# Kernel tuning notes

Measured on AMD Instinct MI355X. Metric: run time of the kernel, lower is better.

## Reference

```python
import jax, jax.numpy as jnp
import numpy as np

VOCAB, ATTR, B = 50257, 16, 256
EMB, ATTR_EMB, HID, ZDIM = 300, 200, 700, 500
MAXLEN = 30
SOS_IDX, EOS_IDX = 1, 2


def setup_inputs() -> dict:
    ks = jax.random.split(jax.random.key(0), 8)
    s = 0.02
    return {
        "z": jax.random.normal(ks[0], (B, ZDIM), jnp.float32),
        "l": jax.random.randint(ks[1], (B,), 0, ATTR),
        "emb_w": jax.random.normal(ks[2], (VOCAB, EMB), jnp.float32) * s,
        "attr_w": jax.random.normal(ks[3], (ATTR, ATTR_EMB), jnp.float32) * s,
        "W_ih": jax.random.normal(ks[4], (3 * HID, EMB), jnp.float32) * s,
        "W_hh": jax.random.normal(ks[5], (3 * HID, HID), jnp.float32) * s,
        "b_ih": jnp.zeros((3 * HID,), jnp.float32),
        "b_hh": jnp.zeros((3 * HID,), jnp.float32),
        "out_w": jax.random.normal(ks[6], (VOCAB, HID), jnp.float32) * s,
        "out_b": jnp.zeros((VOCAB,), jnp.float32),
    }


def gru_cell(x, h, W_ih, W_hh, b_ih, b_hh):
    # PyTorch GRU cell: r,z,n gate ordering
    gi = x @ W_ih.T + b_ih          # (B, 3H)
    gh = h @ W_hh.T + b_hh          # (B, 3H)
    i_r, i_z, i_n = jnp.split(gi, 3, axis=-1)
    h_r, h_z, h_n = jnp.split(gh, 3, axis=-1)
    r = jax.nn.sigmoid(i_r + h_r)
    zg = jax.nn.sigmoid(i_z + h_z)
    n = jnp.tanh(i_n + r * h_n)
    return (1.0 - zg) * n + zg * h


def reference(z, l, emb_w, attr_w, W_ih, W_hh, b_ih, b_hh, out_w, out_b):
    # hidden init: cat([z (B,500), attr_emb(l) (B,200)]) -> (B,700)
    h0 = jnp.concatenate([z, attr_w[l]], axis=-1)
    tok0 = jnp.full((B,), SOS_IDX, jnp.int32)
    keys = jax.random.split(jax.random.key(42), MAXLEN)

    def step(carry, k):
        h, tok = carry
        x = emb_w[tok]                                   # (B,300)
        h = gru_cell(x, h, W_ih, W_hh, b_ih, b_hh)       # (B,700)
        logits = h @ out_w.T + out_b                     # (B,VOCAB)
        # multinomial(softmax(logits), 1).detach()
        nxt = jax.lax.stop_gradient(
            jax.random.categorical(k, logits).astype(jnp.int32))
        return (h, nxt), (h, nxt)

    (h_last, _), (hy_t, y_t) = jax.lax.scan(step, (h0, tok0), keys)
    # final forced-EOS step
    eos = jnp.full((B,), EOS_IDX, jnp.int32)
    h_final = gru_cell(emb_w[eos], h_last, W_ih, W_hh, b_ih, b_hh)
    hy = jnp.concatenate([jnp.transpose(hy_t, (1, 0, 2)), h_final[:, None, :]], axis=1)  # (B,MAXLEN+1,700)
    y = jnp.concatenate([jnp.transpose(y_t, (1, 0)), eos[:, None]], axis=1)              # (B,MAXLEN+1)
    return hy, y
```

## Files before the change

kernel.cpp:

```cpp
#include <hip/hip_runtime.h>
#include <stdint.h>

#define VOCAB 50257
#define B 256
#define EMB 300
#define HID 700
#define G3 2100
#define ZDIM 500
#define ATTR_EMBD 200
#define MAXLEN 30
#define SEQ 31
#define HY_ELEMS (B*SEQ*HID)
#define KP 704
#define NKT 22
#define KIH 320
#define VPAD 50304
#define NVT 393
#define MPAD 2112
#define SOS_IDX 1
#define EOS_IDX 2
#define CHUNK 4096
#define TILE_STRIDE ((size_t)NKT * 2 * CHUNK)

typedef _Float16 half8 __attribute__((ext_vector_type(8)));
typedef _Float16 half4 __attribute__((ext_vector_type(4)));
typedef float f32x4 __attribute__((ext_vector_type(4)));

typedef const __attribute__((address_space(1))) void* gas1_t;
typedef __attribute__((address_space(3))) void* las3_t;
__device__ __forceinline__ void gload_lds16(const void* g, void* l) {
  __builtin_amdgcn_global_load_lds((gas1_t)g, (las3_t)l, 16, 0, 0);
}

__device__ __forceinline__ uint32_t rotl32(uint32_t x, int r) {
  return (x << r) | (x >> (32 - r));
}

__device__ __forceinline__ void threefry2x32(uint32_t k0, uint32_t k1,
                                             uint32_t x0, uint32_t x1,
                                             uint32_t& o0, uint32_t& o1) {
  const uint32_t ks2 = k0 ^ k1 ^ 0x1BD11BDAu;
  x0 += k0; x1 += k1;
#define TF_R4(a, b, c, d)                                     \
  x0 += x1; x1 = rotl32(x1, a); x1 ^= x0;                     \
  x0 += x1; x1 = rotl32(x1, b); x1 ^= x0;                     \
  x0 += x1; x1 = rotl32(x1, c); x1 ^= x0;                     \
  x0 += x1; x1 = rotl32(x1, d); x1 ^= x0;
  TF_R4(13, 15, 26, 6)  x0 += k1;  x1 += ks2 + 1u;
  TF_R4(17, 29, 16, 24) x0 += ks2; x1 += k0 + 2u;
  TF_R4(13, 15, 26, 6)  x0 += k0;  x1 += k1 + 3u;
  TF_R4(17, 29, 16, 24) x0 += k1;  x1 += ks2 + 4u;
  TF_R4(13, 15, 26, 6)  x0 += ks2; x1 += k0 + 5u;
#undef TF_R4
  o0 = x0; o1 = x1;
}

__device__ __forceinline__ unsigned long long gumbel_pack(float s, uint32_t key0,
                                                          uint32_t key1, int b, int v) {
  uint32_t j = (uint32_t)(b * VOCAB + v);
  uint32_t o0, o1;
  threefry2x32(key0, key1, 0u, j, o0, o1);
  uint32_t bits = o0 ^ o1;
  float f = __uint_as_float((bits >> 9) | 0x3f800000u) - 1.0f;
  float u = fmaxf(f, 1.17549435e-38f);
  float g = -logf(-logf(u));
  s += g;
  uint32_t us = __float_as_uint(s);
  us = (us & 0x80000000u) ? ~us : (us | 0x80000000u);
  return ((unsigned long long)us << 32) | (uint32_t)(~(uint32_t)v);
}

struct hl16 { _Float16 hi, lo; };
__device__ __forceinline__ hl16 split16(float val, float scale) {
  float s = val * scale;
  _Float16 h = (_Float16)s;
  hl16 r;
  r.hi = h;
  r.lo = (_Float16)((s - (float)h) * 2048.0f);
  return r;
}

__global__ void k_init(const float* __restrict__ z, const int* __restrict__ l,
                       const float* __restrict__ attr_w, const float* __restrict__ emb_w,
                       float* __restrict__ hbuf0, uint32_t* __restrict__ keys,
                       unsigned long long* __restrict__ slots,
                       int* __restrict__ tok, float* __restrict__ y_out,
                       _Float16* __restrict__ h_hi, _Float16* __restrict__ h_lo,
                       _Float16* __restrict__ ht,
                       _Float16* __restrict__ x0_hi, _Float16* __restrict__ x0_lo,
                       _Float16* __restrict__ xe_hi, _Float16* __restrict__ xe_lo,
                       int full) {
  int idx = blockIdx.x * blockDim.x + threadIdx.x;
  if (idx < B * HID) {
    int b = idx / HID, i = idx % HID;
    float v = (i < ZDIM) ? z[b * ZDIM + i]
                         : attr_w[l[b] * ATTR_EMBD + (i - ZDIM)];
    hbuf0[idx] = v;
    hl16 r = split16(v, 8.0f);
    h_hi[b * KP + i] = r.hi;
    h_lo[b * KP + i] = r.lo;
  }
  if (idx < MAXLEN) {
    uint32_t o0, o1;
    threefry2x32(0u, 42u, 0u, (uint32_t)idx, o0, o1);
    keys[2 * idx] = o0; keys[2 * idx + 1] = o1;
  }
  if (idx < MAXLEN * B) slots[idx] = 0ull;
  if (idx < B) {
    tok[idx] = SOS_IDX;
    tok[31 * B + idx] = EOS_IDX;
    y_out[idx * SEQ + MAXLEN] = 2.0f;
  }
  if (idx < B * 4) {
    int b = idx >> 2, k = HID + (idx & 3);
    h_hi[b * KP + k] = (_Float16)0.0f;
    h_lo[b * KP + k] = (_Float16)0.0f;
    int c = b >> 7, row = b & 127, e = k & 7;
    size_t tb = (size_t)c * TILE_STRIDE + (size_t)21 * 2 * CHUNK
              + (3 * 128 + row) * 8 + e;
    ht[tb] = (_Float16)0.0f;
    ht[tb + CHUNK] = (_Float16)0.0f;
  }
  if (full && idx < KIH) {
    float v0 = (idx < EMB) ? emb_w[SOS_IDX * EMB + idx] : 0.0f;
    float ve = (idx < EMB) ? emb_w[EOS_IDX * EMB + idx] : 0.0f;
    hl16 r0 = split16(v0, 8.0f);
    hl16 re = split16(ve, 8.0f);
    for (int b = 0; b < B; ++b) {
      x0_hi[b * KIH + idx] = r0.hi; x0_lo[b * KIH + idx] = r0.lo;
      xe_hi[b * KIH + idx] = re.hi; xe_lo[b * KIH + idx] = re.lo;
    }
  }
}

__global__ void k_wsplit(const float* __restrict__ out_w, _Float16* __restrict__ wt) {
  size_t idx = (size_t)blockIdx.x * blockDim.x + threadIdx.x;
  if (idx >= (size_t)NVT * NKT * 1024) return;
  int h4 = (int)(idx & 1023);
  int ktp = (int)(idx >> 10);
  int kt = ktp % NKT, p = ktp / NKT;
  int slot4 = h4 >> 1, e0 = (h4 & 1) * 4;
  int kc = slot4 >> 7, row = slot4 & 127;
  int v = p * 128 + row;
  int k = kt * 32 + kc * 8 + e0;
  float x[4];
  if (v < VOCAB && k + 3 < HID) {
    const float4 xv = *(const float4*)&out_w[(size_t)v * HID + k];
    x[0] = xv.x; x[1] = xv.y; x[2] = xv.z; x[3] = xv.w;
  } else {
#pragma unroll
    for (int j = 0; j < 4; ++j)
      x[j] = (v < VOCAB && k + j < HID) ? out_w[(size_t)v * HID + k + j] : 0.0f;
  }
  half4 hi, lo;
#pragma unroll
  for (int j = 0; j < 4; ++j) {
    hl16 r = split16(x[j], 64.0f);
    hi[j] = r.hi; lo[j] = r.lo;
  }
  size_t base = (size_t)p * TILE_STRIDE + (size_t)kt * 2 * CHUNK + slot4 * 8 + e0;
  *(half4*)&wt[base] = hi;
  *(half4*)&wt[base + CHUNK] = lo;
}

__global__ void k_gwsplit(const float* __restrict__ src, _Float16* __restrict__ hi,
                          _Float16* __restrict__ lo, int Msrc, int Ksrc, int Kpad,
                          int tot4) {
  int idx = blockIdx.x * blockDim.x + threadIdx.x;
  if (idx >= tot4) return;
  size_t i4 = (size_t)idx * 4;
  int m = (int)(i4 / Kpad), k = (int)(i4 % Kpad);
  half4 h, l;
#pragma unroll
  for (int j = 0; j < 4; ++j) {
    float x = (m < Msrc && k + j < Ksrc) ? src[(size_t)m * Ksrc + k + j] : 0.0f;
    hl16 r = split16(x, 64.0f);
    h[j] = r.hi; l[j] = r.lo;
  }
  *(half4*)&hi[i4] = h;
  *(half4*)&lo[i4] = l;
}

__global__ __launch_bounds__(256, 4)
void k_gates2(const _Float16* __restrict__ wih_hi, const _Float16* __restrict__ wih_lo,
              const _Float16* __restrict__ whh_hi, const _Float16* __restrict__ whh_lo,
              const _Float16* __restrict__ x_hi, const _Float16* __restrict__ x_lo,
              const _Float16* __restrict__ h_hi, const _Float16* __restrict__ h_lo,
              float* __restrict__ gi, float* __restrict__ gh) {
  const int zz = blockIdx.z;
  const _Float16* __restrict__ Whi = zz ? whh_hi : wih_hi;
  const _Float16* __restrict__ Wlo = zz ? whh_lo : wih_lo;
  const _Float16* __restrict__ Xhi = zz ? h_hi : x_hi;
  const _Float16* __restrict__ Xlo = zz ? h_lo : x_lo;
  const int Kz = zz ? KP : KIH;
  float* __restrict__ out = zz ? gh : gi;

  const int jbase = blockIdx.x * 64;
  const int bbase = blockIdx.y * 64;
  __shared__ float4 lds[2][4][256];
  const int tid = threadIdx.x, lane = tid & 63, wid = tid >> 6;
  const int wj = wid >> 1, wb2 = wid & 1;
  const size_t wrow = (size_t)(jbase + lane) * Kz;
  const size_t xrow = (size_t)(bbase + lane) * Kz;

  f32x4 acc_h[2][2], acc_x[2][2];
#pragma unroll
  for (int i = 0; i < 2; ++i)
#pragma unroll
    for (int j = 0; j < 2; ++j) { acc_h[i][j] = (f32x4)0.0f; acc_x[i][j] = (f32x4)0.0f; }

#define GSTAGE(bf, k0)                                                   \
  {                                                                      \
    gload_lds16(Whi + wrow + (k0) + wid * 8, &lds[bf][0][wid * 64]);     \
    gload_lds16(Wlo + wrow + (k0) + wid * 8, &lds[bf][1][wid * 64]);     \
    gload_lds16(Xhi + xrow + (k0) + wid * 8, &lds[bf][2][wid * 64]);     \
    gload_lds16(Xlo + xrow + (k0) + wid * 8, &lds[bf][3][wid * 64]);     \
  }

  const int nt = Kz / 32;
  GSTAGE(0, 0)
  for (int kt = 0; kt < nt; ++kt) {
    const int cur = kt & 1;
    __syncthreads();
    if (kt + 1 < nt) GSTAGE(cur ^ 1, (kt + 1) * 32)
    const int kcf = (lane >> 4) * 64 + (lane & 15);
    half8 a_hi[2], a_lo[2];
#pragma unroll
    for (int fv = 0; fv < 2; ++fv) {
      int s = kcf + wj * 32 + fv * 16;
      a_hi[fv] = *(const half8*)&lds[cur][0][s];
      a_lo[fv] = *(const half8*)&lds[cur][1][s];
    }
#pragma unroll
    for (int fb = 0; fb < 2; ++fb) {
      int s = kcf + wb2 * 32 + fb * 16;
      half8 b_hi = *(const half8*)&lds[cur][2][s];
      half8 b_lo = *(const half8*)&lds[cur][3][s];
#pragma unroll
      for (int fv = 0; fv < 2; ++fv) {
        acc_h[fv][fb] = __builtin_amdgcn_mfma_f32_16x16x32_f16(a_hi[fv], b_hi,
                                                               acc_h[fv][fb], 0, 0, 0);
        acc_x[fv][fb] = __builtin_amdgcn_mfma_f32_16x16x32_f16(a_hi[fv], b_lo,
                                                               acc_x[fv][fb], 0, 0, 0);
        acc_x[fv][fb] = __builtin_amdgcn_mfma_f32_16x16x32_f16(a_lo[fv], b_hi,
                                                               acc_x[fv][fb], 0, 0, 0);
      }
    }
  }
#undef GSTAGE

  const float c1 = 1.0f / 2048.0f, c2 = 1.0f / 512.0f;
#pragma unroll
  for (int fb = 0; fb < 2; ++fb) {
    const int b = bbase + wb2 * 32 + fb * 16 + (lane & 15);
#pragma unroll
    for (int fv = 0; fv < 2; ++fv) {
#pragma unroll
      for (int r = 0; r < 4; ++r) {
        int j = jbase + wj * 32 + fv * 16 + (lane >> 4) * 4 + r;
        if (j < G3)
          out[b * G3 + j] = (acc_h[fv][fb][r] + acc_x[fv][fb][r] * c1) * c2;
      }
    }
  }
}

__global__ void k_gates(const float* __restrict__ W_ih, const float* __restrict__ W_hh,
                        const float* __restrict__ emb_w, const float* __restrict__ hprev,
                        const int* __restrict__ tok,
                        float* __restrict__ gi, float* __restrict__ gh) {
  const int zz = blockIdx.z;
  const float* __restrict__ W = zz ? W_hh : W_ih;
  const int K = zz ? HID : EMB;
  float* __restrict__ out = zz ? gh : gi;
  __shared__ float w_lds[20][36];
  __shared__ float xh_lds[20][36];
  const int jbase = blockIdx.x * 32;
  const int bbase = blockIdx.y * 32;
  const int tid = threadIdx.x;
  const int tj = tid % 16, tb = tid / 16;
  float a00 = 0.f, a01 = 0.f, a10 = 0.f, a11 = 0.f;
  for (int k0 = 0; k0 < K; k0 += 20) {
    for (int idx = tid; idx < 640; idx += 256) {
      int col = idx / 20, kk = idx % 20;
      int j = jbase + col;
      w_lds[kk][col] = (j < G3) ? W[j * K + k0 + kk] : 0.0f;
      int b = bbase + col;
      float xv;
      if (zz) xv = hprev[b * HID + k0 + kk];
      else    xv = emb_w[tok[b] * EMB + k0 + kk];
      xh_lds[kk][col] = xv;
    }
    __syncthreads();
#pragma unroll
    for (int kk = 0; kk < 20; ++kk) {
      float w0 = w_lds[kk][tj * 2], w1 = w_lds[kk][tj * 2 + 1];
      float h0 = xh_lds[kk][tb * 2], h1 = xh_lds[kk][tb * 2 + 1];
      a00 += w0 * h0; a01 += w0 * h1;
      a10 += w1 * h0; a11 += w1 * h1;
    }
    __syncthreads();
  }
  int j0 = jbase + tj * 2, b0 = bbase + tb * 2;
  if (j0 < G3)     { out[b0 * G3 + j0] = a00;     out[(b0 + 1) * G3 + j0] = a01; }
  if (j0 + 1 < G3) { out[b0 * G3 + j0 + 1] = a10; out[(b0 + 1) * G3 + j0 + 1] = a11; }
}

__global__ void k_hnew(const float* __restrict__ gi, const float* __restrict__ gh,
                       const float* __restrict__ b_ih, const float* __restrict__ b_hh,
                       const float* __restrict__ hprev, float* __restrict__ hnext,
                       float* __restrict__ hy, _Float16* __restrict__ h_hi,
                       _Float16* __restrict__ h_lo, _Float16* __restrict__ ht, int t) {
  int idx = blockIdx.x * blockDim.x + threadIdx.x;
  if (idx >= B * HID) return;
  int b = idx / HID, i = idx % HID;
  float ir = gi[b * G3 + i]            + b_ih[i];
  float iz = gi[b * G3 + HID + i]      + b_ih[HID + i];
  float in_ = gi[b * G3 + 2 * HID + i] + b_ih[2 * HID + i];
  float hr = gh[b * G3 + i]            + b_hh[i];
  float hz = gh[b * G3 + HID + i]      + b_hh[HID + i];
  float hn = gh[b * G3 + 2 * HID + i]  + b_hh[2 * HID + i];
  float r  = 1.0f / (1.0f + expf(-(ir + hr)));
  float zg = 1.0f / (1.0f + expf(-(iz + hz)));
  float n  = tanhf(in_ + r * hn);
  float h  = (1.0f - zg) * n + zg * hprev[idx];
  hnext[idx] = h;
  hy[(size_t)b * SEQ * HID + (size_t)t * HID + i] = h;
  hl16 rr = split16(h, 8.0f);
  h_hi[b * KP + i] = rr.hi;
  h_lo[b * KP + i] = rr.lo;
  int c = b >> 7, row = b & 127;
  size_t tb = (size_t)c * TILE_STRIDE + (size_t)(i >> 5) * 2 * CHUNK
            + ((((i >> 3) & 3) * 128 + row) * 8) + (i & 7);
  ht[tb] = rr.hi;
  ht[tb + CHUNK] = rr.lo;
}

__global__ __launch_bounds__(256, 2)
void k_logits2(const _Float16* __restrict__ wt, const _Float16* __restrict__ ht,
               const float* __restrict__ out_b, const uint32_t* __restrict__ keys,
               unsigned long long* __restrict__ slot, int t) {
  const int bid = blockIdx.x;
  const int xcd = bid & 7, li = bid >> 3;
  const int p = xcd * 50 + (li >> 1);
  if (p >= NVT) return;
  const int c = li & 1;
  const int vbase = p * 128, bbase = c * 128;

  __shared__ float4 lds[2][4][512];
  const int tid = threadIdx.x;
  const int lane = tid & 63;
  const int wid = tid >> 6;
  const int wv = wid >> 1, wb = wid & 1;

  const int part = wid & 1;
  const _Float16* tile_base = (wid < 2) ? (wt + (size_t)p * TILE_STRIDE)
                                        : (ht + (size_t)c * TILE_STRIDE);

  f32x4 acc_h[4][4];
  f32x4 acc_x[4][4];
#pragma unroll
  for (int i = 0; i < 4; ++i)
#pragma unroll
    for (int j = 0; j < 4; ++j) { acc_h[i][j] = (f32x4)0.0f; acc_x[i][j] = (f32x4)0.0f; }

#define LSTAGE(bf, kt)                                                          \
  {                                                                             \
    const _Float16* sb =                                                        \
        tile_base + ((size_t)(kt) * 2 + part) * CHUNK + lane * 8;               \
    _Pragma("unroll")                                                           \
    for (int i = 0; i < 8; ++i)                                                 \
      gload_lds16(sb + i * 512, &lds[bf][wid][i * 64]);                         \
  }

  LSTAGE(0, 0)
  for (int kt = 0; kt < NKT; ++kt) {
    const int cur = kt & 1;
    __syncthreads();
    if (kt + 1 < NKT) LSTAGE(cur ^ 1, kt + 1)
    const int kcf = (lane >> 4) * 128 + (lane & 15);
    half8 a_hi[4], a_lo[4];
#pragma unroll
    for (int fv = 0; fv < 4; ++fv) {
      int s = kcf + wv * 64 + fv * 16;
      a_hi[fv] = *(const half8*)&lds[cur][0][s];
      a_lo[fv] = *(const half8*)&lds[cur][1][s];
    }
#pragma unroll
    for (int fb = 0; fb < 4; ++fb) {
      int s = kcf + wb * 64 + fb * 16;
      half8 b_hi = *(const half8*)&lds[cur][2][s];
      half8 b_lo = *(const half8*)&lds[cur][3][s];
#pragma unroll
      for (int fv = 0; fv < 4; ++fv) {
        acc_h[fv][fb] = __builtin_amdgcn_mfma_f32_16x16x32_f16(a_hi[fv], b_hi,
                                                               acc_h[fv][fb], 0, 0, 0);
        acc_x[fv][fb] = __builtin_amdgcn_mfma_f32_16x16x32_f16(a_hi[fv], b_lo,
                                                               acc_x[fv][fb], 0, 0, 0);
        acc_x[fv][fb] = __builtin_amdgcn_mfma_f32_16x16x32_f16(a_lo[fv], b_hi,
                                                               acc_x[fv][fb], 0, 0, 0);
      }
    }
  }
#undef LSTAGE

  const uint32_t key0 = keys[2 * t], key1 = keys[2 * t + 1];
  const float c1 = 1.0f / 2048.0f, c2 = 1.0f / 512.0f;
#pragma unroll
  for (int fb = 0; fb < 4; ++fb) {
    const int b = bbase + wb * 64 + fb * 16 + (lane & 15);
    unsigned long long best = 0ull;
#pragma unroll
    for (int fv = 0; fv < 4; ++fv) {
#pragma unroll
      for (int r = 0; r < 4; ++r) {
        int v = vbase + wv * 64 + fv * 16 + (lane >> 4) * 4 + r;
        if (v < VOCAB) {
          float s = (acc_h[fv][fb][r] + acc_x[fv][fb][r] * c1) * c2 + out_b[v];
          unsigned long long cand = gumbel_pack(s, key0, key1, b, v);
          if (cand > best) best = cand;
        }
      }
    }
    unsigned long long o;
    o = __shfl_xor(best, 16, 64); if (o > best) best = o;
    o = __shfl_xor(best, 32, 64); if (o > best) best = o;
    if ((lane >> 4) == 0) atomicMax(&slot[b], best);
  }
}

#define WPITCH 68
#define HPITCH 260
__global__ __launch_bounds__(256)
void k_logits_f32(const float* __restrict__ h, const float* __restrict__ out_w,
                  const float* __restrict__ out_b, const uint32_t* __restrict__ keys,
                  unsigned long long* __restrict__ slot, int t) {
  __shared__ float w_lds[20][WPITCH];
  __shared__ float h_lds[20][HPITCH];
  const int vbase = blockIdx.x * 64;
  const int tid = threadIdx.x;
  const int tv = tid % 8, tb = tid / 8;
  float acc[8][8];
#pragma unroll
  for (int i = 0; i < 8; ++i)
#pragma unroll
    for (int j = 0; j < 8; ++j) acc[i][j] = 0.f;

  for (int k0 = 0; k0 < HID; k0 += 20) {
    for (int idx = tid; idx < 64 * 20; idx += 256) {
      int vv = idx / 20, kk = idx % 20;
      int v = vbase + vv;
      w_lds[kk][vv] = (v < VOCAB) ? out_w[(size_t)v * HID + k0 + kk] : 0.0f;
    }
    for (int idx = tid; idx < 256 * 20; idx += 256) {
      int bb = idx / 20, kk = idx % 20;
      h_lds[kk][bb] = h[bb * HID + k0 + kk];
    }
    __syncthreads();
#pragma unroll
    for (int kk = 0; kk < 20; ++kk) {
      float wv[8], hv[8];
      *(float4*)&wv[0] = *(const float4*)&w_lds[kk][tv * 8];
      *(float4*)&wv[4] = *(const float4*)&w_lds[kk][tv * 8 + 4];
      *(float4*)&hv[0] = *(const float4*)&h_lds[kk][tb * 8];
      *(float4*)&hv[4] = *(const float4*)&h_lds[kk][tb * 8 + 4];
#pragma unroll
      for (int iv = 0; iv < 8; ++iv)
#pragma unroll
        for (int ib = 0; ib < 8; ++ib) acc[iv][ib] += wv[iv] * hv[ib];
    }
    __syncthreads();
  }

  const uint32_t key0 = keys[2 * t], key1 = keys[2 * t + 1];
#pragma unroll
  for (int ib = 0; ib < 8; ++ib) {
    const int b = tb * 8 + ib;
    unsigned long long best = 0ull;
#pragma unroll
    for (int iv = 0; iv < 8; ++iv) {
      int v = vbase + tv * 8 + iv;
      if (v >= VOCAB) continue;
      unsigned long long cand = gumbel_pack(acc[iv][ib] + out_b[v], key0, key1, b, v);
      if (cand > best) best = cand;
    }
#pragma unroll
    for (int off = 1; off < 8; off <<= 1) {
      unsigned long long other = __shfl_xor(best, off, 64);
      if (other > best) best = other;
    }
    if (tv == 0) atomicMax(&slot[b], best);
  }
}

__global__ void k_tok2(const unsigned long long* __restrict__ slot,
                       const float* __restrict__ emb_w,
                       int* __restrict__ tok_next, float* __restrict__ y_out,
                       _Float16* __restrict__ xc_hi, _Float16* __restrict__ xc_lo,
                       int t, int full) {
  const int b = blockIdx.x;
  const int c = threadIdx.x;
  unsigned long long p = slot[b];
  uint32_t v = ~((uint32_t)(p & 0xFFFFFFFFull));
  if (c == 0) {
    tok_next[b] = (int)v;
    y_out[b * SEQ + t] = (float)v;
  }
  if (!full) return;
  if (c < 75) {
    float4 xv = *(const float4*)&emb_w[(size_t)v * EMB + c * 4];
    half4 hi, lo;
    hl16 r0 = split16(xv.x, 8.0f); hi[0] = r0.hi; lo[0] = r0.lo;
    hl16 r1 = split16(xv.y, 8.0f); hi[1] = r1.hi; lo[1] = r1.lo;
    hl16 r2 = split16(xv.z, 8.0f); hi[2] = r2.hi; lo[2] = r2.lo;
    hl16 r3 = split16(xv.w, 8.0f); hi[3] = r3.hi; lo[3] = r3.lo;
    *(half4*)&xc_hi[b * KIH + c * 4] = hi;
    *(half4*)&xc_lo[b * KIH + c * 4] = lo;
  } else if (c < 80) {
    *(half4*)&xc_hi[b * KIH + c * 4] = (half4)(_Float16)0.0f;
    *(half4*)&xc_lo[b * KIH + c * 4] = (half4)(_Float16)0.0f;
  }
}

extern "C" void kernel_launch(void* const* d_in, const int* in_sizes, int n_in,
                              void* d_out, int out_size, void* d_ws, size_t ws_size,
                              hipStream_t stream) {
  const float* z      = (const float*)d_in[0];
  const int*   l      = (const int*)  d_in[1];
  const float* emb_w  = (const float*)d_in[2];
  const float* attr_w = (const float*)d_in[3];
  const float* W_ih   = (const float*)d_in[4];
  const float* W_hh   = (const float*)d_in[5];
  const float* b_ih   = (const float*)d_in[6];
  const float* b_hh   = (const float*)d_in[7];
  const float* out_w  = (const float*)d_in[8];
  const float* out_b  = (const float*)d_in[9];

  float* hy    = (float*)d_out;
  float* y_out = (float*)d_out + HY_ELEMS;

  char* ws = (char*)d_ws;
  size_t off = 0;
  uint32_t* keys            = (uint32_t*)(ws + off);           off += 256;
  unsigned long long* slots = (unsigned long long*)(ws + off); off += (size_t)MAXLEN * B * 8;
  int* tokbuf               = (int*)(ws + off);                off += (size_t)32 * B * 4;
  float* hbuf               = (float*)(ws + off);              off += (size_t)2 * B * HID * 4;
  float* gi                 = (float*)(ws + off);              off += (size_t)B * G3 * 4;
  float* gh                 = (float*)(ws + off);              off += (size_t)B * G3 * 4;
  _Float16* h_hi            = (_Float16*)(ws + off);           off += (size_t)B * KP * 2;
  _Float16* h_lo            = (_Float16*)(ws + off);           off += (size_t)B * KP * 2;
  _Float16* ht              = (_Float16*)(ws + off);           off += (size_t)2 * TILE_STRIDE * 2;
  _Float16* wt              = (_Float16*)(ws + off);           off += (size_t)NVT * TILE_STRIDE * 2;
  const size_t tier1_end = off;
  _Float16* wih_hi          = (_Float16*)(ws + off);           off += (size_t)MPAD * KIH * 2;
  _Float16* wih_lo          = (_Float16*)(ws + off);           off += (size_t)MPAD * KIH * 2;
  _Float16* whh_hi          = (_Float16*)(ws + off);           off += (size_t)MPAD * KP * 2;
  _Float16* whh_lo          = (_Float16*)(ws + off);           off += (size_t)MPAD * KP * 2;
  _Float16* x0_hi           = (_Float16*)(ws + off);           off += (size_t)B * KIH * 2;
  _Float16* x0_lo           = (_Float16*)(ws + off);           off += (size_t)B * KIH * 2;
  _Float16* xe_hi           = (_Float16*)(ws + off);           off += (size_t)B * KIH * 2;
  _Float16* xe_lo           = (_Float16*)(ws + off);           off += (size_t)B * KIH * 2;
  _Float16* xc_hi           = (_Float16*)(ws + off);           off += (size_t)B * KIH * 2;
  _Float16* xc_lo           = (_Float16*)(ws + off);           off += (size_t)B * KIH * 2;
  const size_t tier2_end = off;
  const int tier = (ws_size >= tier2_end) ? 2 : ((ws_size >= tier1_end) ? 1 : 0);

  k_init<<<(B * HID + 255) / 256, 256, 0, stream>>>(
      z, l, attr_w, emb_w, hbuf, keys, slots, tokbuf, y_out, h_hi, h_lo, ht,
      x0_hi, x0_lo, xe_hi, xe_lo, (tier == 2) ? 1 : 0);

  if (tier >= 1) {
    size_t tot = (size_t)NVT * NKT * 1024;
    k_wsplit<<<(int)((tot + 255) / 256), 256, 0, stream>>>(out_w, wt);
  }
  if (tier == 2) {
    int tih = MPAD * KIH / 4, thh = MPAD * KP / 4;
    k_gwsplit<<<(tih + 255) / 256, 256, 0, stream>>>(W_ih, wih_hi, wih_lo, G3, EMB, KIH, tih);
    k_gwsplit<<<(thh + 255) / 256, 256, 0, stream>>>(W_hh, whh_hi, whh_lo, G3, HID, KP, thh);
  }

  for (int t = 0; t <= MAXLEN; ++t) {
    float* hprev = hbuf + (t % 2) * B * HID;
    float* hnext = hbuf + ((t + 1) % 2) * B * HID;

    if (tier == 2) {
      const _Float16* xh = (t == 0) ? x0_hi : ((t == MAXLEN) ? xe_hi : xc_hi);
      const _Float16* xl = (t == 0) ? x0_lo : ((t == MAXLEN) ? xe_lo : xc_lo);
      dim3 g2(33, 4, 2);
      k_gates2<<<g2, 256, 0, stream>>>(wih_hi, wih_lo, whh_hi, whh_lo,
                                       xh, xl, h_hi, h_lo, gi, gh);
    } else {
      const int* tok_t = tokbuf + ((t == MAXLEN) ? 31 : t) * B;
      dim3 ggrid(66, 8, 2);
      k_gates<<<ggrid, 256, 0, stream>>>(W_ih, W_hh, emb_w, hprev, tok_t, gi, gh);
    }
    k_hnew<<<(B * HID + 255) / 256, 256, 0, stream>>>(gi, gh, b_ih, b_hh, hprev,
                                                      hnext, hy, h_hi, h_lo, ht, t);
    if (t < MAXLEN) {
      if (tier >= 1) {
        k_logits2<<<800, 256, 0, stream>>>(wt, ht, out_b, keys,
                                           slots + (size_t)t * B, t);
      } else {
        k_logits_f32<<<(VOCAB + 63) / 64, 256, 0, stream>>>(hnext, out_w, out_b, keys,
                                                            slots + (size_t)t * B, t);
      }
      k_tok2<<<B, 128, 0, stream>>>(slots + (size_t)t * B, emb_w,
                                    tokbuf + (t + 1) * B, y_out, xc_hi, xc_lo,
                                    t, (tier == 2) ? 1 : 0);
    }
  }
}
```

Measured before the change: 4.025 ms.

## Load logits MFMA operands directly from global into registers, drop LDS staging

The logits GEMM kernel stops staging weight and hidden tiles through double-buffered shared memory with per-iteration block barriers. Each wave now loads its own A and B fragments straight from global memory into registers, ping-ponging two register sets for the weight fragments to overlap loads with MFMA work. This removes the LDS round trip and the __syncthreads per k-tile. The cost is redundant global and L2 loads across waves, since each weight fragment is read by two waves and each h fragment by two, and higher register pressure that may hurt occupancy.

```diff
diff --git a/kernel.cpp b/kernel.cpp
--- a/kernel.cpp
+++ b/kernel.cpp
@@ -337,7 +337,7 @@
 }
 
 __global__ __launch_bounds__(256, 2)
-void k_logits2(const _Float16* __restrict__ wt, const _Float16* __restrict__ ht,
+void k_logits3(const _Float16* __restrict__ wt, const _Float16* __restrict__ ht,
                const float* __restrict__ out_b, const uint32_t* __restrict__ keys,
                unsigned long long* __restrict__ slot, int t) {
   const int bid = blockIdx.x;
@@ -347,15 +347,16 @@
   const int c = li & 1;
   const int vbase = p * 128, bbase = c * 128;
 
-  __shared__ float4 lds[2][4][512];
   const int tid = threadIdx.x;
   const int lane = tid & 63;
   const int wid = tid >> 6;
   const int wv = wid >> 1, wb = wid & 1;
 
-  const int part = wid & 1;
-  const _Float16* tile_base = (wid < 2) ? (wt + (size_t)p * TILE_STRIDE)
-                                        : (ht + (size_t)c * TILE_STRIDE);
+  const _Float16* __restrict__ wp = wt + (size_t)p * TILE_STRIDE;
+  const _Float16* __restrict__ hp = ht + (size_t)c * TILE_STRIDE;
+  const int kcf = (lane >> 4) * 128 + (lane & 15);
+  const int aoff = (kcf + wv * 64) * 8;
+  const int boff = (kcf + wb * 64) * 8;
 
   f32x4 acc_h[4][4];
   f32x4 acc_x[4][4];
@@ -364,45 +365,53 @@
 #pragma unroll
     for (int j = 0; j < 4; ++j) { acc_h[i][j] = (f32x4)0.0f; acc_x[i][j] = (f32x4)0.0f; }
 
-#define LSTAGE(bf, kt)                                                          \
-  {                                                                             \
-    const _Float16* sb =                                                        \
-        tile_base + ((size_t)(kt) * 2 + part) * CHUNK + lane * 8;               \
-    _Pragma("unroll")                                                           \
-    for (int i = 0; i < 8; ++i)                                                 \
-      gload_lds16(sb + i * 512, &lds[bf][wid][i * 64]);                         \
-  }
-
-  LSTAGE(0, 0)
-  for (int kt = 0; kt < NKT; ++kt) {
-    const int cur = kt & 1;
-    __syncthreads();
-    if (kt + 1 < NKT) LSTAGE(cur ^ 1, kt + 1)
-    const int kcf = (lane >> 4) * 128 + (lane & 15);
-    half8 a_hi[4], a_lo[4];
-#pragma unroll
-    for (int fv = 0; fv < 4; ++fv) {
-      int s = kcf + wv * 64 + fv * 16;
-      a_hi[fv] = *(const half8*)&lds[cur][0][s];
-      a_lo[fv] = *(const half8*)&lds[cur][1][s];
-    }
-#pragma unroll
-    for (int fb = 0; fb < 4; ++fb) {
-      int s = kcf + wb * 64 + fb * 16;
-      half8 b_hi = *(const half8*)&lds[cur][2][s];
-      half8 b_lo = *(const half8*)&lds[cur][3][s];
-#pragma unroll
-      for (int fv = 0; fv < 4; ++fv) {
-        acc_h[fv][fb] = __builtin_amdgcn_mfma_f32_16x16x32_f16(a_hi[fv], b_hi,
-                                                               acc_h[fv][fb], 0, 0, 0);
-        acc_x[fv][fb] = __builtin_amdgcn_mfma_f32_16x16x32_f16(a_hi[fv], b_lo,
-                                                               acc_x[fv][fb], 0, 0, 0);
-        acc_x[fv][fb] = __builtin_amdgcn_mfma_f32_16x16x32_f16(a_lo[fv], b_hi,
-                                                               acc_x[fv][fb], 0, 0, 0);
-      }
-    }
-  }
-#undef LSTAGE
+  half8 wA_hi[4], wA_lo[4], wB_hi[4], wB_lo[4], hC_hi[4], hC_lo[4];
+
+#define LOADW(WH, WL, ktv)                                                \
+  {                                                                       \
+    const _Float16* bw = wp + (size_t)(ktv) * (2 * CHUNK);                \
+    _Pragma("unroll")                                                     \
+    for (int fv = 0; fv < 4; ++fv) {                                      \
+      WH[fv] = *(const half8*)(bw + aoff + fv * 128);                     \
+      WL[fv] = *(const half8*)(bw + CHUNK + aoff + fv * 128);             \
+    }                                                                     \
+  }
+#define LOADH(ktv)                                                        \
+  {                                                                       \
+    const _Float16* bh = hp + (size_t)(ktv) * (2 * CHUNK);                \
+    _Pragma("unroll")                                                     \
+    for (int fb = 0; fb < 4; ++fb) {                                      \
+      hC_hi[fb] = *(const half8*)(bh + boff + fb * 128);                  \
+      hC_lo[fb] = *(const half8*)(bh + CHUNK + boff + fb * 128);          \
+    }                                                                     \
+  }
+#define MFMAB(AH, AL)                                                     \
+  _Pragma("unroll")                                                       \
+  for (int fb = 0; fb < 4; ++fb) {                                        \
+    _Pragma("unroll")                                                     \
+    for (int fv = 0; fv < 4; ++fv) {                                      \
+      acc_h[fv][fb] = __builtin_amdgcn_mfma_f32_16x16x32_f16(             \
+          AH[fv], hC_hi[fb], acc_h[fv][fb], 0, 0, 0);                     \
+      acc_x[fv][fb] = __builtin_amdgcn_mfma_f32_16x16x32_f16(             \
+          AH[fv], hC_lo[fb], acc_x[fv][fb], 0, 0, 0);                     \
+      acc_x[fv][fb] = __builtin_amdgcn_mfma_f32_16x16x32_f16(             \
+          AL[fv], hC_hi[fb], acc_x[fv][fb], 0, 0, 0);                     \
+    }                                                                     \
+  }
+
+  LOADW(wA_hi, wA_lo, 0)
+#pragma unroll 1
+  for (int kt = 0; kt < NKT; kt += 2) {
+    LOADH(kt)
+    LOADW(wB_hi, wB_lo, kt + 1)
+    MFMAB(wA_hi, wA_lo)
+    LOADH(kt + 1)
+    if (kt + 2 < NKT) LOADW(wA_hi, wA_lo, kt + 2)
+    MFMAB(wB_hi, wB_lo)
+  }
+#undef LOADW
+#undef LOADH
+#undef MFMAB
 
   const uint32_t key0 = keys[2 * t], key1 = keys[2 * t + 1];
   const float c1 = 1.0f / 2048.0f, c2 = 1.0f / 512.0f;
@@ -598,7 +607,7 @@
                                                       hnext, hy, h_hi, h_lo, ht, t);
     if (t < MAXLEN) {
       if (tier >= 1) {
-        k_logits2<<<800, 256, 0, stream>>>(wt, ht, out_b, keys,
+        k_logits3<<<800, 256, 0, stream>>>(wt, ht, out_b, keys,
                                            slots + (size_t)t * B, t);
       } else {
         k_logits_f32<<<(VOCAB + 63) / 64, 256, 0, stream>>>(hnext, out_w, out_b, keys,
```

Result: slower. 4.125 ms (+2.5%).

## Retile logits GEMM into 128x32 work items with persistent multi-item blocks

Applied to the files above, without the earlier changes.

Replaces the 128x128 vocab-by-batch logits tile kernel with one that processes three 128x32 items per block, staging only weight tiles in LDS while loading the small hidden-state fragments directly from global memory. The hidden-state tile layout is changed to 32-row batch chunks to match, and occupancy is raised to 4 blocks per SM. The Gumbel sampling also switches to fast __logf. Total weight traffic grows because each weight tile is now read once per 32-row batch chunk instead of once per 128-row chunk, which it relies on L2 to absorb. The fast log may change sampled tokens slightly.

```diff
diff --git a/kernel.cpp b/kernel.cpp
--- a/kernel.cpp
+++ b/kernel.cpp
@@ -21,6 +21,10 @@
 #define EOS_IDX 2
 #define CHUNK 4096
 #define TILE_STRIDE ((size_t)NKT * 2 * CHUNK)
+#define HT_KT 2048
+#define HT_C ((size_t)NKT * HT_KT)
+#define NITEMS 3144
+#define NBLK 1048
 
 typedef _Float16 half8 __attribute__((ext_vector_type(8)));
 typedef _Float16 half4 __attribute__((ext_vector_type(4)));
@@ -63,7 +67,7 @@
   uint32_t bits = o0 ^ o1;
   float f = __uint_as_float((bits >> 9) | 0x3f800000u) - 1.0f;
   float u = fmaxf(f, 1.17549435e-38f);
-  float g = -logf(-logf(u));
+  float g = -__logf(-__logf(u));
   s += g;
   uint32_t us = __float_as_uint(s);
   us = (us & 0x80000000u) ? ~us : (us | 0x80000000u);
@@ -115,11 +119,11 @@
     int b = idx >> 2, k = HID + (idx & 3);
     h_hi[b * KP + k] = (_Float16)0.0f;
     h_lo[b * KP + k] = (_Float16)0.0f;
-    int c = b >> 7, row = b & 127, e = k & 7;
-    size_t tb = (size_t)c * TILE_STRIDE + (size_t)21 * 2 * CHUNK
-              + (3 * 128 + row) * 8 + e;
+    int c = b >> 5, row = b & 31;
+    size_t tb = (size_t)c * HT_C + (size_t)21 * HT_KT + (size_t)(3 * 32 + row) * 8
+              + (k & 7);
     ht[tb] = (_Float16)0.0f;
-    ht[tb + CHUNK] = (_Float16)0.0f;
+    ht[tb + 1024] = (_Float16)0.0f;
   }
   if (full && idx < KIH) {
     float v0 = (idx < EMB) ? emb_w[SOS_IDX * EMB + idx] : 0.0f;
@@ -329,104 +333,106 @@
   hl16 rr = split16(h, 8.0f);
   h_hi[b * KP + i] = rr.hi;
   h_lo[b * KP + i] = rr.lo;
-  int c = b >> 7, row = b & 127;
-  size_t tb = (size_t)c * TILE_STRIDE + (size_t)(i >> 5) * 2 * CHUNK
-            + ((((i >> 3) & 3) * 128 + row) * 8) + (i & 7);
+  int c = b >> 5, row = b & 31;
+  size_t tb = (size_t)c * HT_C + (size_t)(i >> 5) * HT_KT
+            + (size_t)((((i >> 3) & 3) * 32 + row) * 8) + (i & 7);
   ht[tb] = rr.hi;
-  ht[tb + CHUNK] = rr.lo;
-}
-
-__global__ __launch_bounds__(256, 2)
-void k_logits2(const _Float16* __restrict__ wt, const _Float16* __restrict__ ht,
+  ht[tb + 1024] = rr.lo;
+}
+
+__global__ __launch_bounds__(256, 4)
+void k_logits4(const _Float16* __restrict__ wt, const _Float16* __restrict__ ht,
                const float* __restrict__ out_b, const uint32_t* __restrict__ keys,
                unsigned long long* __restrict__ slot, int t) {
-  const int bid = blockIdx.x;
-  const int xcd = bid & 7, li = bid >> 3;
-  const int p = xcd * 50 + (li >> 1);
-  if (p >= NVT) return;
-  const int c = li & 1;
-  const int vbase = p * 128, bbase = c * 128;
-
-  __shared__ float4 lds[2][4][512];
+  __shared__ float4 ldsw[2][1024];
   const int tid = threadIdx.x;
   const int lane = tid & 63;
   const int wid = tid >> 6;
-  const int wv = wid >> 1, wb = wid & 1;
-
-  const int part = wid & 1;
-  const _Float16* tile_base = (wid < 2) ? (wt + (size_t)p * TILE_STRIDE)
-                                        : (ht + (size_t)c * TILE_STRIDE);
-
-  f32x4 acc_h[4][4];
-  f32x4 acc_x[4][4];
-#pragma unroll
-  for (int i = 0; i < 4; ++i)
-#pragma unroll
-    for (int j = 0; j < 4; ++j) { acc_h[i][j] = (f32x4)0.0f; acc_x[i][j] = (f32x4)0.0f; }
-
-#define LSTAGE(bf, kt)                                                          \
-  {                                                                             \
-    const _Float16* sb =                                                        \
-        tile_base + ((size_t)(kt) * 2 + part) * CHUNK + lane * 8;               \
-    _Pragma("unroll")                                                           \
-    for (int i = 0; i < 8; ++i)                                                 \
-      gload_lds16(sb + i * 512, &lds[bf][wid][i * 64]);                         \
-  }
-
-  LSTAGE(0, 0)
-  for (int kt = 0; kt < NKT; ++kt) {
-    const int cur = kt & 1;
-    __syncthreads();
-    if (kt + 1 < NKT) LSTAGE(cur ^ 1, kt + 1)
-    const int kcf = (lane >> 4) * 128 + (lane & 15);
-    half8 a_hi[4], a_lo[4];
-#pragma unroll
-    for (int fv = 0; fv < 4; ++fv) {
-      int s = kcf + wv * 64 + fv * 16;
-      a_hi[fv] = *(const half8*)&lds[cur][0][s];
-      a_lo[fv] = *(const half8*)&lds[cur][1][s];
-    }
-#pragma unroll
-    for (int fb = 0; fb < 4; ++fb) {
-      int s = kcf + wb * 64 + fb * 16;
-      half8 b_hi = *(const half8*)&lds[cur][2][s];
-      half8 b_lo = *(const half8*)&lds[cur][3][s];
-#pragma unroll
-      for (int fv = 0; fv < 4; ++fv) {
-        acc_h[fv][fb] = __builtin_amdgcn_mfma_f32_16x16x32_f16(a_hi[fv], b_hi,
-                                                               acc_h[fv][fb], 0, 0, 0);
-        acc_x[fv][fb] = __builtin_amdgcn_mfma_f32_16x16x32_f16(a_hi[fv], b_lo,
-                                                               acc_x[fv][fb], 0, 0, 0);
-        acc_x[fv][fb] = __builtin_amdgcn_mfma_f32_16x16x32_f16(a_lo[fv], b_hi,
-                                                               acc_x[fv][fb], 0, 0, 0);
-      }
-    }
-  }
-#undef LSTAGE
+  const int work = (blockIdx.x & 7) * 131 + (blockIdx.x >> 3);
 
   const uint32_t key0 = keys[2 * t], key1 = keys[2 * t + 1];
   const float c1 = 1.0f / 2048.0f, c2 = 1.0f / 512.0f;
-#pragma unroll
-  for (int fb = 0; fb < 4; ++fb) {
-    const int b = bbase + wb * 64 + fb * 16 + (lane & 15);
-    unsigned long long best = 0ull;
-#pragma unroll
-    for (int fv = 0; fv < 4; ++fv) {
-#pragma unroll
-      for (int r = 0; r < 4; ++r) {
-        int v = vbase + wv * 64 + fv * 16 + (lane >> 4) * 4 + r;
-        if (v < VOCAB) {
-          float s = (acc_h[fv][fb][r] + acc_x[fv][fb][r] * c1) * c2 + out_b[v];
-          unsigned long long cand = gumbel_pack(s, key0, key1, b, v);
-          if (cand > best) best = cand;
+
+  const int wrow = (lane >> 4) * 128 + (lane & 15) + wid * 32;
+  const int hrow = ((lane >> 4) * 32 + (lane & 15)) * 8;
+
+#define STAGE4(bf, ktv)                                                        \
+  {                                                                            \
+    _Pragma("unroll")                                                          \
+    for (int j = 0; j < 4; ++j) {                                              \
+      const int s = wid * 4 + j;                                               \
+      gload_lds16(wp + (size_t)(ktv) * (2 * CHUNK) + (size_t)(s >> 3) * CHUNK  \
+                      + (s & 7) * 512 + lane * 8,                              \
+                  &ldsw[bf][s * 64]);                                          \
+    }                                                                          \
+  }
+
+  for (int it = 0; it < 3; ++it) {
+    const int item = work * 3 + it;
+    const int p = item >> 3, cc = item & 7;
+    const int vbase = p * 128, bbase = cc * 32;
+    const _Float16* __restrict__ wp = wt + (size_t)p * TILE_STRIDE;
+    const _Float16* __restrict__ hq0 = ht + (size_t)cc * HT_C;
+
+    f32x4 acc_h[2][2], acc_x[2][2];
+#pragma unroll
+    for (int i = 0; i < 2; ++i)
+#pragma unroll
+      for (int j = 0; j < 2; ++j) { acc_h[i][j] = (f32x4)0.0f; acc_x[i][j] = (f32x4)0.0f; }
+
+    STAGE4(0, 0)
+    for (int kt = 0; kt < NKT; ++kt) {
+      const int cur = kt & 1;
+      __syncthreads();
+      const _Float16* hq = hq0 + (size_t)kt * HT_KT;
+      half8 hC_hi[2], hC_lo[2];
+      hC_hi[0] = *(const half8*)(hq + hrow);
+      hC_hi[1] = *(const half8*)(hq + hrow + 128);
+      hC_lo[0] = *(const half8*)(hq + 1024 + hrow);
+      hC_lo[1] = *(const half8*)(hq + 1024 + hrow + 128);
+      if (kt + 1 < NKT) STAGE4(cur ^ 1, kt + 1)
+      half8 wA_hi[2], wA_lo[2];
+      wA_hi[0] = *(const half8*)&ldsw[cur][wrow];
+      wA_hi[1] = *(const half8*)&ldsw[cur][wrow + 16];
+      wA_lo[0] = *(const half8*)&ldsw[cur][wrow + 512];
+      wA_lo[1] = *(const half8*)&ldsw[cur][wrow + 512 + 16];
+#pragma unroll
+      for (int fb = 0; fb < 2; ++fb) {
+#pragma unroll
+        for (int fv = 0; fv < 2; ++fv) {
+          acc_h[fv][fb] = __builtin_amdgcn_mfma_f32_16x16x32_f16(
+              wA_hi[fv], hC_hi[fb], acc_h[fv][fb], 0, 0, 0);
+          acc_x[fv][fb] = __builtin_amdgcn_mfma_f32_16x16x32_f16(
+              wA_hi[fv], hC_lo[fb], acc_x[fv][fb], 0, 0, 0);
+          acc_x[fv][fb] = __builtin_amdgcn_mfma_f32_16x16x32_f16(
+              wA_lo[fv], hC_hi[fb], acc_x[fv][fb], 0, 0, 0);
         }
       }
     }
-    unsigned long long o;
-    o = __shfl_xor(best, 16, 64); if (o > best) best = o;
-    o = __shfl_xor(best, 32, 64); if (o > best) best = o;
-    if ((lane >> 4) == 0) atomicMax(&slot[b], best);
-  }
+
+#pragma unroll
+    for (int fb = 0; fb < 2; ++fb) {
+      const int b = bbase + fb * 16 + (lane & 15);
+      unsigned long long best = 0ull;
+#pragma unroll
+      for (int fv = 0; fv < 2; ++fv) {
+#pragma unroll
+        for (int r = 0; r < 4; ++r) {
+          int v = vbase + wid * 32 + fv * 16 + (lane >> 4) * 4 + r;
+          if (v < VOCAB) {
+            float s = (acc_h[fv][fb][r] + acc_x[fv][fb][r] * c1) * c2 + out_b[v];
+            unsigned long long cand = gumbel_pack(s, key0, key1, b, v);
+            if (cand > best) best = cand;
+          }
+        }
+      }
+      unsigned long long o;
+      o = __shfl_xor(best, 16, 64); if (o > best) best = o;
+      o = __shfl_xor(best, 32, 64); if (o > best) best = o;
+      if ((lane >> 4) == 0) atomicMax(&slot[b], best);
+    }
+  }
+#undef STAGE4
 }
 
 #define WPITCH 68
@@ -549,7 +555,7 @@
   float* gh                 = (float*)(ws + off);              off += (size_t)B * G3 * 4;
   _Float16* h_hi            = (_Float16*)(ws + off);           off += (size_t)B * KP * 2;
   _Float16* h_lo            = (_Float16*)(ws + off);           off += (size_t)B * KP * 2;
-  _Float16* ht              = (_Float16*)(ws + off);           off += (size_t)2 * TILE_STRIDE * 2;
+  _Float16* ht              = (_Float16*)(ws + off);           off += (size_t)8 * HT_C * 2;
   _Float16* wt              = (_Float16*)(ws + off);           off += (size_t)NVT * TILE_STRIDE * 2;
   const size_t tier1_end = off;
   _Float16* wih_hi          = (_Float16*)(ws + off);           off += (size_t)MPAD * KIH * 2;
@@ -598,8 +604,8 @@
                                                       hnext, hy, h_hi, h_lo, ht, t);
     if (t < MAXLEN) {
       if (tier >= 1) {
-        k_logits2<<<800, 256, 0, stream>>>(wt, ht, out_b, keys,
-                                           slots + (size_t)t * B, t);
+        k_logits4<<<NBLK, 256, 0, stream>>>(wt, ht, out_b, keys,
+                                            slots + (size_t)t * B, t);
       } else {
         k_logits_f32<<<(VOCAB + 63) / 64, 256, 0, stream>>>(hnext, out_w, out_b, keys,
                                                             slots + (size_t)t * B, t);
```

Measured after the change: 5.136 ms. 1.28x slower.

## Restructure logits GEMM with register-held weights, smaller tiles and single accumulator

Applied to the files above, without the earlier changes.

Replaces the logits kernel with a version that splits each vocab tile into halves across more blocks and keeps weight fragments in registers loaded directly from global memory. Only the hidden-state tile is staged in LDS, with an explicit double buffer. The hi/lo split drops its 2048 scaling so all three MFMA products can accumulate into one register set, halving accumulator pressure and allowing four blocks per CU. Fast __logf replaces logf in the Gumbel sampling. The risks are fp16 underflow of the unscaled low part, which reduces precision, and small deviations from the fast log that could flip sampled tokens.

```diff
diff --git a/kernel.cpp b/kernel.cpp
--- a/kernel.cpp
+++ b/kernel.cpp
@@ -21,6 +21,8 @@
 #define EOS_IDX 2
 #define CHUNK 4096
 #define TILE_STRIDE ((size_t)NKT * 2 * CHUNK)
+#define NIT5 1572
+#define NBLK5 1576
 
 typedef _Float16 half8 __attribute__((ext_vector_type(8)));
 typedef _Float16 half4 __attribute__((ext_vector_type(4)));
@@ -63,7 +65,7 @@
   uint32_t bits = o0 ^ o1;
   float f = __uint_as_float((bits >> 9) | 0x3f800000u) - 1.0f;
   float u = fmaxf(f, 1.17549435e-38f);
-  float g = -logf(-logf(u));
+  float g = -__logf(-__logf(u));
   s += g;
   uint32_t us = __float_as_uint(s);
   us = (us & 0x80000000u) ? ~us : (us | 0x80000000u);
@@ -76,7 +78,7 @@
   _Float16 h = (_Float16)s;
   hl16 r;
   r.hi = h;
-  r.lo = (_Float16)((s - (float)h) * 2048.0f);
+  r.lo = (_Float16)(s - (float)h);
   return r;
 }
 
@@ -203,11 +205,11 @@
   const size_t wrow = (size_t)(jbase + lane) * Kz;
   const size_t xrow = (size_t)(bbase + lane) * Kz;
 
-  f32x4 acc_h[2][2], acc_x[2][2];
+  f32x4 acc[2][2];
 #pragma unroll
   for (int i = 0; i < 2; ++i)
 #pragma unroll
-    for (int j = 0; j < 2; ++j) { acc_h[i][j] = (f32x4)0.0f; acc_x[i][j] = (f32x4)0.0f; }
+    for (int j = 0; j < 2; ++j) acc[i][j] = (f32x4)0.0f;
 
 #define GSTAGE(bf, k0)                                                   \
   {                                                                      \
@@ -238,18 +240,18 @@
       half8 b_lo = *(const half8*)&lds[cur][3][s];
 #pragma unroll
       for (int fv = 0; fv < 2; ++fv) {
-        acc_h[fv][fb] = __builtin_amdgcn_mfma_f32_16x16x32_f16(a_hi[fv], b_hi,
-                                                               acc_h[fv][fb], 0, 0, 0);
-        acc_x[fv][fb] = __builtin_amdgcn_mfma_f32_16x16x32_f16(a_hi[fv], b_lo,
-                                                               acc_x[fv][fb], 0, 0, 0);
-        acc_x[fv][fb] = __builtin_amdgcn_mfma_f32_16x16x32_f16(a_lo[fv], b_hi,
-                                                               acc_x[fv][fb], 0, 0, 0);
+        acc[fv][fb] = __builtin_amdgcn_mfma_f32_16x16x32_f16(a_hi[fv], b_hi,
+                                                             acc[fv][fb], 0, 0, 0);
+        acc[fv][fb] = __builtin_amdgcn_mfma_f32_16x16x32_f16(a_hi[fv], b_lo,
+                                                             acc[fv][fb], 0, 0, 0);
+        acc[fv][fb] = __builtin_amdgcn_mfma_f32_16x16x32_f16(a_lo[fv], b_hi,
+                                                             acc[fv][fb], 0, 0, 0);
       }
     }
   }
 #undef GSTAGE
 
-  const float c1 = 1.0f / 2048.0f, c2 = 1.0f / 512.0f;
+  const float c2 = 1.0f / 512.0f;
 #pragma unroll
   for (int fb = 0; fb < 2; ++fb) {
     const int b = bbase + wb2 * 32 + fb * 16 + (lane & 15);
@@ -258,8 +260,7 @@
 #pragma unroll
       for (int r = 0; r < 4; ++r) {
         int j = jbase + wj * 32 + fv * 16 + (lane >> 4) * 4 + r;
-        if (j < G3)
-          out[b * G3 + j] = (acc_h[fv][fb][r] + acc_x[fv][fb][r] * c1) * c2;
+        if (j < G3) out[b * G3 + j] = acc[fv][fb][r] * c2;
       }
     }
   }
@@ -336,87 +337,96 @@
   ht[tb + CHUNK] = rr.lo;
 }
 
-__global__ __launch_bounds__(256, 2)
-void k_logits2(const _Float16* __restrict__ wt, const _Float16* __restrict__ ht,
+__global__ __launch_bounds__(256, 4)
+void k_logits5(const _Float16* __restrict__ wt, const _Float16* __restrict__ ht,
                const float* __restrict__ out_b, const uint32_t* __restrict__ keys,
                unsigned long long* __restrict__ slot, int t) {
-  const int bid = blockIdx.x;
-  const int xcd = bid & 7, li = bid >> 3;
-  const int p = xcd * 50 + (li >> 1);
-  if (p >= NVT) return;
-  const int c = li & 1;
-  const int vbase = p * 128, bbase = c * 128;
-
-  __shared__ float4 lds[2][4][512];
-  const int tid = threadIdx.x;
-  const int lane = tid & 63;
-  const int wid = tid >> 6;
+  const int item = (blockIdx.x & 7) * 197 + (blockIdx.x >> 3);
+  if (item >= NIT5) return;
+  const int p = item >> 2, vh = (item >> 1) & 1, c = item & 1;
+
+  __shared__ float4 ldsh[2][1024];
+  const int tid = threadIdx.x, lane = tid & 63, wid = tid >> 6;
   const int wv = wid >> 1, wb = wid & 1;
-
-  const int part = wid & 1;
-  const _Float16* tile_base = (wid < 2) ? (wt + (size_t)p * TILE_STRIDE)
-                                        : (ht + (size_t)c * TILE_STRIDE);
-
-  f32x4 acc_h[4][4];
-  f32x4 acc_x[4][4];
-#pragma unroll
-  for (int i = 0; i < 4; ++i)
-#pragma unroll
-    for (int j = 0; j < 4; ++j) { acc_h[i][j] = (f32x4)0.0f; acc_x[i][j] = (f32x4)0.0f; }
-
-#define LSTAGE(bf, kt)                                                          \
-  {                                                                             \
-    const _Float16* sb =                                                        \
-        tile_base + ((size_t)(kt) * 2 + part) * CHUNK + lane * 8;               \
-    _Pragma("unroll")                                                           \
-    for (int i = 0; i < 8; ++i)                                                 \
-      gload_lds16(sb + i * 512, &lds[bf][wid][i * 64]);                         \
-  }
-
-  LSTAGE(0, 0)
-  for (int kt = 0; kt < NKT; ++kt) {
-    const int cur = kt & 1;
+  const int lq = lane >> 4, lr = lane & 15;
+
+  const _Float16* __restrict__ wp = wt + (size_t)p * TILE_STRIDE;
+  const _Float16* __restrict__ hp = ht + (size_t)c * TILE_STRIDE;
+
+  const int wslot = lq * 128 + vh * 64 + wv * 32 + lr;
+  const int hslot = lq * 128 + wb * 64 + lr;
+
+  f32x4 acc[2][4];
+#pragma unroll
+  for (int i = 0; i < 2; ++i)
+#pragma unroll
+    for (int j = 0; j < 4; ++j) acc[i][j] = (f32x4)0.0f;
+
+  half8 wA[4], wB[4];
+
+#define LOADW(W, ktv)                                                         \
+  {                                                                           \
+    const _Float16* bw = wp + (size_t)(ktv) * (2 * CHUNK);                    \
+    _Pragma("unroll")                                                         \
+    for (int fv = 0; fv < 2; ++fv) {                                          \
+      W[fv * 2 + 0] = *(const half8*)(bw + (wslot + fv * 16) * 8);            \
+      W[fv * 2 + 1] = *(const half8*)(bw + CHUNK + (wslot + fv * 16) * 8);    \
+    }                                                                         \
+  }
+#define STAGEH(bf, ktv)                                                       \
+  {                                                                           \
+    const _Float16* bh = hp + (size_t)(ktv) * (2 * CHUNK);                    \
+    _Pragma("unroll")                                                         \
+    for (int j = 0; j < 4; ++j)                                               \
+      gload_lds16(bh + (j * 256 + wid * 64 + lane) * 8,                       \
+                  &ldsh[bf][j * 256 + wid * 64]);                             \
+  }
+#define COMPUTE(bf, W)                                                        \
+  _Pragma("unroll")                                                           \
+  for (int fb = 0; fb < 4; ++fb) {                                            \
+    half8 hhi = *(const half8*)&ldsh[bf][hslot + fb * 16];                    \
+    half8 hlo = *(const half8*)&ldsh[bf][512 + hslot + fb * 16];              \
+    _Pragma("unroll")                                                         \
+    for (int fv = 0; fv < 2; ++fv) {                                          \
+      acc[fv][fb] = __builtin_amdgcn_mfma_f32_16x16x32_f16(                   \
+          W[fv * 2 + 0], hhi, acc[fv][fb], 0, 0, 0);                          \
+      acc[fv][fb] = __builtin_amdgcn_mfma_f32_16x16x32_f16(                   \
+          W[fv * 2 + 0], hlo, acc[fv][fb], 0, 0, 0);                          \
+      acc[fv][fb] = __builtin_amdgcn_mfma_f32_16x16x32_f16(                   \
+          W[fv * 2 + 1], hhi, acc[fv][fb], 0, 0, 0);                          \
+    }                                                                         \
+  }
+
+  LOADW(wA, 0)
+  STAGEH(0, 0)
+  __syncthreads();
+#pragma unroll 1
+  for (int kt = 0; kt < NKT; kt += 2) {
+    if (kt + 1 < NKT) { STAGEH(1, kt + 1) LOADW(wB, kt + 1) }
+    COMPUTE(0, wA)
     __syncthreads();
-    if (kt + 1 < NKT) LSTAGE(cur ^ 1, kt + 1)
-    const int kcf = (lane >> 4) * 128 + (lane & 15);
-    half8 a_hi[4], a_lo[4];
-#pragma unroll
-    for (int fv = 0; fv < 4; ++fv) {
-      int s = kcf + wv * 64 + fv * 16;
-      a_hi[fv] = *(const half8*)&lds[cur][0][s];
-      a_lo[fv] = *(const half8*)&lds[cur][1][s];
-    }
-#pragma unroll
-    for (int fb = 0; fb < 4; ++fb) {
-      int s = kcf + wb * 64 + fb * 16;
-      half8 b_hi = *(const half8*)&lds[cur][2][s];
-      half8 b_lo = *(const half8*)&lds[cur][3][s];
-#pragma unroll
-      for (int fv = 0; fv < 4; ++fv) {
-        acc_h[fv][fb] = __builtin_amdgcn_mfma_f32_16x16x32_f16(a_hi[fv], b_hi,
-                                                               acc_h[fv][fb], 0, 0, 0);
-        acc_x[fv][fb] = __builtin_amdgcn_mfma_f32_16x16x32_f16(a_hi[fv], b_lo,
-                                                               acc_x[fv][fb], 0, 0, 0);
-        acc_x[fv][fb] = __builtin_amdgcn_mfma_f32_16x16x32_f16(a_lo[fv], b_hi,
-                                                               acc_x[fv][fb], 0, 0, 0);
-      }
-    }
-  }
-#undef LSTAGE
+    if (kt + 2 < NKT) { STAGEH(0, kt + 2) LOADW(wA, kt + 2) }
+    COMPUTE(1, wB)
+    __syncthreads();
+  }
+#undef LOADW
+#undef STAGEH
+#undef COMPUTE
 
   const uint32_t key0 = keys[2 * t], key1 = keys[2 * t + 1];
-  const float c1 = 1.0f / 2048.0f, c2 = 1.0f / 512.0f;
+  const float c2 = 1.0f / 512.0f;
+  const int vbase0 = p * 128 + vh * 64 + wv * 32;
 #pragma unroll
   for (int fb = 0; fb < 4; ++fb) {
-    const int b = bbase + wb * 64 + fb * 16 + (lane & 15);
+    const int b = c * 128 + wb * 64 + fb * 16 + lr;
     unsigned long long best = 0ull;
 #pragma unroll
-    for (int fv = 0; fv < 4; ++fv) {
+    for (int fv = 0; fv < 2; ++fv) {
 #pragma unroll
       for (int r = 0; r < 4; ++r) {
-        int v = vbase + wv * 64 + fv * 16 + (lane >> 4) * 4 + r;
+        int v = vbase0 + fv * 16 + lq * 4 + r;
         if (v < VOCAB) {
-          float s = (acc_h[fv][fb][r] + acc_x[fv][fb][r] * c1) * c2 + out_b[v];
+          float s = acc[fv][fb][r] * c2 + out_b[v];
           unsigned long long cand = gumbel_pack(s, key0, key1, b, v);
           if (cand > best) best = cand;
         }
@@ -425,7 +435,7 @@
     unsigned long long o;
     o = __shfl_xor(best, 16, 64); if (o > best) best = o;
     o = __shfl_xor(best, 32, 64); if (o > best) best = o;
-    if ((lane >> 4) == 0) atomicMax(&slot[b], best);
+    if (lq == 0) atomicMax(&slot[b], best);
   }
 }
 
@@ -598,8 +608,8 @@
                                                       hnext, hy, h_hi, h_lo, ht, t);
     if (t < MAXLEN) {
       if (tier >= 1) {
-        k_logits2<<<800, 256, 0, stream>>>(wt, ht, out_b, keys,
-                                           slots + (size_t)t * B, t);
+        k_logits5<<<NBLK5, 256, 0, stream>>>(wt, ht, out_b, keys,
+                                             slots + (size_t)t * B, t);
       } else {
         k_logits_f32<<<(VOCAB + 63) / 64, 256, 0, stream>>>(hnext, out_w, out_b, keys,
                                                             slots + (size_t)t * B, t);
```

New measurement: 3.659 ms. 9.1% less time.
